# Optimization experiments

Measured on AMD Instinct MI355X. Metric: run time of the kernel, lower is better.

Reference implementation:

```python
import jax, jax.numpy as jnp
import numpy as np

C = 128
SHAPE = (1, C, 48, 48, 48)  # (N, C, D, H, W)
FILTERS = (1, 3, 3, 3, 1)
INIT_SCALE = 10.0
TAIL_MASS = 1e-9
LIKELIHOOD_BOUND = 1e-9


def setup_inputs() -> dict:
    key = jax.random.key(0)
    ks = jax.random.split(key, 8)
    x = jax.random.normal(ks[0], SHAPE, jnp.float32) * 3.0
    noise = jax.random.uniform(ks[1], SHAPE, jnp.float32)  # shifted to [-0.5,0.5) inside reference
    scale = INIT_SCALE ** (1.0 / (len(FILTERS) - 1))
    inp = {"x": x, "noise": noise}
    for i in range(4):
        init_m = float(np.log(np.expm1(1.0 / scale / FILTERS[i + 1])))
        inp[f"m{i}"] = jnp.full((C, FILTERS[i + 1], FILTERS[i]), init_m, jnp.float32)
        inp[f"b{i}"] = jax.random.uniform(ks[2 + i], (C, FILTERS[i + 1], 1), jnp.float32, -0.5, 0.5)
        if i < 3:
            inp[f"f{i}"] = jnp.zeros((C, FILTERS[i + 1], 1), jnp.float32)
    # quantiles init: [-init_scale, 0, init_scale] per channel, shape (C,1,3)
    inp["quantiles"] = jnp.tile(
        jnp.array([[[-INIT_SCALE, 0.0, INIT_SCALE]]], jnp.float32), (C, 1, 1)
    )
    return inp


def _logits_cumulative(z, mats, biases, factors, stop_gradient=False):
    # z: (C, 1, B); per-channel tiny 4-layer CDF MLP
    sg = jax.lax.stop_gradient if stop_gradient else (lambda t: t)
    for i in range(4):
        m = sg(jax.nn.softplus(mats[i]))          # (C, f_out, f_in)
        z = jnp.matmul(m, z) + sg(biases[i])      # (C, f_out, B)
        if i < 3:
            z = z + sg(jnp.tanh(factors[i])) * jnp.tanh(z)
    return z


def reference(x, noise, m0, m1, m2, m3, b0, b1, b2, b3, f0, f1, f2, quantiles):
    mats = [m0, m1, m2, m3]
    biases = [b0, b1, b2, b3]
    factors = [f0, f1, f2]

    # quantize_mode == 'noise': additive uniform(-0.5, 0.5) noise
    outputs = x + (noise - 0.5)

    n, c, d, h, w = outputs.shape
    z = jnp.transpose(outputs, (1, 0, 2, 3, 4)).reshape(c, 1, -1)  # (C,1,B)
    lower = _logits_cumulative(z - 0.5, mats, biases, factors)
    upper = _logits_cumulative(z + 0.5, mats, biases, factors)
    sign = -jax.lax.stop_gradient(jnp.sign(lower + upper))
    likelihood = jnp.abs(jax.nn.sigmoid(sign * upper) - jax.nn.sigmoid(sign * lower))
    likelihood = jnp.transpose(likelihood.reshape(c, n, d, h, w), (1, 0, 2, 3, 4))
    likelihood = jnp.maximum(likelihood, LIKELIHOOD_BOUND)  # Low_bound forward

    t = float(np.log(2.0 / TAIL_MASS - 1.0))
    target = jnp.array([-t, 0.0, t], jnp.float32)
    logits_q = _logits_cumulative(quantiles, mats, biases, factors, stop_gradient=True)
    quantiles_loss = jnp.sum(jnp.abs(logits_q - target))

    return outputs, likelihood, quantiles_loss
```

## Files before the change

kernel.cpp:

```cpp
#include <hip/hip_runtime.h>
#include <math.h>

#define NCH      128
#define SPATIAL  110592
#define NV4      3538944
#define CV4      27648
#define THREADS  256
#define GRID     2048

#define QT 21.416413017506358f

typedef float v4f __attribute__((ext_vector_type(4)));

__device__ __forceinline__ float frcp(float x){ return __builtin_amdgcn_rcpf(x); }
__device__ __forceinline__ float ftanh(float x){ return 1.0f - 2.0f*frcp(__expf(2.0f*x) + 1.0f); }
__device__ __forceinline__ float fsig(float x){ return frcp(1.0f + __expf(-x)); }
__device__ __forceinline__ float fsoftplus(float x){ return fmaxf(x, 0.0f) + log1pf(__expf(-fabsf(x))); }

struct Params {
    float w0[3], w1[9], w2[9], w3[3];
    float t0[3], t1[3], t2[3];
    float B0[3], B1[3], B2[3], B3;
};

__device__ __forceinline__ Params load_params(int c,
    const float* __restrict__ m0, const float* __restrict__ b0, const float* __restrict__ f0,
    const float* __restrict__ m1, const float* __restrict__ b1, const float* __restrict__ f1,
    const float* __restrict__ m2, const float* __restrict__ b2, const float* __restrict__ f2,
    const float* __restrict__ m3, const float* __restrict__ b3)
{
    Params P;
    #pragma unroll
    for (int k=0;k<3;k++) P.w0[k]=fsoftplus(m0[c*3+k]);
    #pragma unroll
    for (int k=0;k<9;k++) P.w1[k]=fsoftplus(m1[c*9+k]);
    #pragma unroll
    for (int k=0;k<9;k++) P.w2[k]=fsoftplus(m2[c*9+k]);
    #pragma unroll
    for (int k=0;k<3;k++) P.w3[k]=fsoftplus(m3[c*3+k]);
    #pragma unroll
    for (int k=0;k<3;k++) P.t0[k]=ftanh(f0[c*3+k]);
    #pragma unroll
    for (int k=0;k<3;k++) P.t1[k]=ftanh(f1[c*3+k]);
    #pragma unroll
    for (int k=0;k<3;k++) P.t2[k]=ftanh(f2[c*3+k]);
    #pragma unroll
    for (int k=0;k<3;k++) P.B0[k]=b0[c*3+k];
    #pragma unroll
    for (int k=0;k<3;k++) P.B1[k]=b1[c*3+k];
    #pragma unroll
    for (int k=0;k<3;k++) P.B2[k]=b2[c*3+k];
    P.B3 = b3[c];
    return P;
}

template<bool USE_F>
__device__ __forceinline__ float eval_mlp(float z, const Params& P){
    float h0 = fmaf(P.w0[0], z, P.B0[0]);
    float h1 = fmaf(P.w0[1], z, P.B0[1]);
    float h2 = fmaf(P.w0[2], z, P.B0[2]);
    if (USE_F){
        h0 = fmaf(P.t0[0], ftanh(h0), h0);
        h1 = fmaf(P.t0[1], ftanh(h1), h1);
        h2 = fmaf(P.t0[2], ftanh(h2), h2);
    }
    float g0 = fmaf(P.w1[0],h0, fmaf(P.w1[1],h1, fmaf(P.w1[2],h2, P.B1[0])));
    float g1 = fmaf(P.w1[3],h0, fmaf(P.w1[4],h1, fmaf(P.w1[5],h2, P.B1[1])));
    float g2 = fmaf(P.w1[6],h0, fmaf(P.w1[7],h1, fmaf(P.w1[8],h2, P.B1[2])));
    if (USE_F){
        g0 = fmaf(P.t1[0], ftanh(g0), g0);
        g1 = fmaf(P.t1[1], ftanh(g1), g1);
        g2 = fmaf(P.t1[2], ftanh(g2), g2);
    }
    h0 = fmaf(P.w2[0],g0, fmaf(P.w2[1],g1, fmaf(P.w2[2],g2, P.B2[0])));
    h1 = fmaf(P.w2[3],g0, fmaf(P.w2[4],g1, fmaf(P.w2[5],g2, P.B2[1])));
    h2 = fmaf(P.w2[6],g0, fmaf(P.w2[7],g1, fmaf(P.w2[8],g2, P.B2[2])));
    if (USE_F){
        h0 = fmaf(P.t2[0], ftanh(h0), h0);
        h1 = fmaf(P.t2[1], ftanh(h1), h1);
        h2 = fmaf(P.t2[2], ftanh(h2), h2);
    }
    return fmaf(P.w3[0],h0, fmaf(P.w3[1],h1, fmaf(P.w3[2],h2, P.B3)));
}

__device__ __forceinline__ float lik_from_logits(float lo, float hi){
    float su = lo + hi;
    float s  = (su > 0.0f) ? -1.0f : ((su < 0.0f) ? 1.0f : 0.0f);
    float a  = fsig(s*hi);
    float b  = fsig(s*lo);
    return fmaxf(fabsf(a - b), 1e-9f);
}

__global__ __launch_bounds__(384) void eb_prep(
    const float* __restrict__ m0, const float* __restrict__ b0, const float* __restrict__ f0,
    const float* __restrict__ m1, const float* __restrict__ b1, const float* __restrict__ f1,
    const float* __restrict__ m2, const float* __restrict__ b2, const float* __restrict__ f2,
    const float* __restrict__ m3, const float* __restrict__ b3,
    const float* __restrict__ q, float* __restrict__ loss,
    float2* __restrict__ ab, int* __restrict__ flag)
{
    const int tid = threadIdx.x;
    const int c = tid / 3;
    const int j = tid - c*3;

    Params P = load_params(c, m0,b0,f0, m1,b1,f1, m2,b2,f2, m3,b3);

    bool anyf = false;
    #pragma unroll
    for (int k=0;k<3;k++)
        anyf = anyf || (P.t0[k]!=0.0f) || (P.t1[k]!=0.0f) || (P.t2[k]!=0.0f);

    __shared__ int sf;
    if (tid == 0) sf = 0;
    __syncthreads();
    if (anyf) sf = 1;

    float z      = q[c*3 + j];
    float logit  = eval_mlp<true>(z, P);
    float target = (j==0) ? -QT : ((j==1) ? 0.0f : QT);
    float diff   = fabsf(logit - target);

    #pragma unroll
    for (int off = 32; off > 0; off >>= 1)
        diff += __shfl_down(diff, off, 64);

    __shared__ float red[6];
    if ((tid & 63) == 0) red[tid >> 6] = diff;
    __syncthreads();
    if (tid == 0){
        float s = 0.0f;
        #pragma unroll
        for (int i = 0; i < 6; i++) s += red[i];
        *loss = s;
        *flag = sf;
    }

    if (j == 0){
        float B = eval_mlp<false>(0.0f, P);
        float A = eval_mlp<false>(1.0f, P) - B;
        ab[c] = make_float2(A, B - 0.5f*A);
    }
}

__global__ __launch_bounds__(THREADS) void eb_main(
    const float* __restrict__ x, const float* __restrict__ noise,
    const float* __restrict__ m0, const float* __restrict__ b0, const float* __restrict__ f0,
    const float* __restrict__ m1, const float* __restrict__ b1, const float* __restrict__ f1,
    const float* __restrict__ m2, const float* __restrict__ b2, const float* __restrict__ f2,
    const float* __restrict__ m3, const float* __restrict__ b3,
    const float2* __restrict__ ab, const int* __restrict__ flag,
    float* __restrict__ out, float* __restrict__ lik)
{
    __shared__ float sA[NCH], sBl[NCH];
    __shared__ int sflag;
    const int tid = threadIdx.x;
    if (tid < NCH){ float2 v = ab[tid]; sA[tid] = v.x; sBl[tid] = v.y; }
    if (tid == 0) sflag = *flag;
    __syncthreads();
    const bool use_f = (sflag != 0);

    const v4f* __restrict__ x4 = (const v4f*)x;
    const v4f* __restrict__ n4 = (const v4f*)noise;
    v4f* __restrict__ o4 = (v4f*)out;
    v4f* __restrict__ l4 = (v4f*)lik;

    int i = blockIdx.x*THREADS + tid;
    const int stride = GRID*THREADS;

    if (!use_f){
        v4f xa = x4[i], na = n4[i];
        while (true){
            const int inext = i + stride;
            const bool vnext = inext < NV4;
            v4f xb, nb;
            if (vnext){ xb = x4[inext]; nb = n4[inext]; }

            const int c = i / CV4;
            const float A  = sA[c];
            const float Bl = sBl[c];

            v4f ov, lv;
            #pragma unroll
            for (int e = 0; e < 4; ++e){
                float o  = xa[e] + na[e] - 0.5f;
                float lo = fmaf(A, o, Bl);
                float hi = lo + A;
                ov[e] = o;
                lv[e] = lik_from_logits(lo, hi);
            }
            __builtin_nontemporal_store(ov, o4 + i);
            __builtin_nontemporal_store(lv, l4 + i);

            if (!vnext) break;
            i = inext; xa = xb; na = nb;
        }
    } else {
        for (; i < NV4; i += stride){
            const int c = i / CV4;
            Params P = load_params(c, m0,b0,f0, m1,b1,f1, m2,b2,f2, m3,b3);
            v4f xv = x4[i], nv = n4[i];
            v4f ov, lv;
            #pragma unroll
            for (int e = 0; e < 4; ++e){
                float o  = xv[e] + nv[e] - 0.5f;
                float lo = eval_mlp<true>(o - 0.5f, P);
                float hi = eval_mlp<true>(o + 0.5f, P);
                ov[e] = o;
                lv[e] = lik_from_logits(lo, hi);
            }
            __builtin_nontemporal_store(ov, o4 + i);
            __builtin_nontemporal_store(lv, l4 + i);
        }
    }
}

extern "C" void kernel_launch(void* const* d_in, const int* in_sizes, int n_in,
                              void* d_out, int out_size, void* d_ws, size_t ws_size,
                              hipStream_t stream) {
    const float* x  = (const float*)d_in[0];
    const float* nz = (const float*)d_in[1];
    const float* m0 = (const float*)d_in[2];
    const float* b0 = (const float*)d_in[3];
    const float* f0 = (const float*)d_in[4];
    const float* m1 = (const float*)d_in[5];
    const float* b1 = (const float*)d_in[6];
    const float* f1 = (const float*)d_in[7];
    const float* m2 = (const float*)d_in[8];
    const float* b2 = (const float*)d_in[9];
    const float* f2 = (const float*)d_in[10];
    const float* m3 = (const float*)d_in[11];
    const float* b3 = (const float*)d_in[12];
    const float* qq = (const float*)d_in[13];

    float* out  = (float*)d_out;
    float* lik  = out + (size_t)NCH*SPATIAL;
    float* loss = lik + (size_t)NCH*SPATIAL;

    float2* ab  = (float2*)d_ws;
    int*   flag = (int*)((char*)d_ws + NCH*sizeof(float2));

    eb_prep<<<1, 384, 0, stream>>>(m0,b0,f0, m1,b1,f1, m2,b2,f2, m3,b3, qq, loss, ab, flag);
    eb_main<<<GRID, THREADS, 0, stream>>>(x, nz, m0,b0,f0, m1,b1,f1, m2,b2,f2, m3,b3,
                                          ab, flag, out, lik);
}
```

Baseline: 231.4 us.

## Issue all tile loads up front with fixed per-block channel mapping

Replaces the grid-stride loop with a fixed 8-tile-per-thread scheme over 1728 blocks. All 16 vector loads are issued before any compute to raise memory-level parallelism. Each block's channels are known at compile time from the block index, which removes the shared-memory staging of per-channel coefficients and the block barrier. It raises register pressure and hardcodes the shape-dependent index mapping.

After: 238.4 us. 1.03x slower.

```diff
diff --git a/kernel.cpp b/kernel.cpp
--- a/kernel.cpp
+++ b/kernel.cpp
@@ -6,7 +6,9 @@
 #define NV4      3538944
 #define CV4      27648
 #define THREADS  256
-#define GRID     2048
+#define GRID     1728
+#define KTILES   8
+#define STRIDE   442368
 
 #define QT 21.416413017506358f
 
@@ -151,58 +153,57 @@
     const float2* __restrict__ ab, const int* __restrict__ flag,
     float* __restrict__ out, float* __restrict__ lik)
 {
-    __shared__ float sA[NCH], sBl[NCH];
-    __shared__ int sflag;
-    const int tid = threadIdx.x;
-    if (tid < NCH){ float2 v = ab[tid]; sA[tid] = v.x; sBl[tid] = v.y; }
-    if (tid == 0) sflag = *flag;
-    __syncthreads();
-    const bool use_f = (sflag != 0);
+    const int tid   = threadIdx.x;
+    const int cbase = blockIdx.x / 108;
+    const int i0    = blockIdx.x*THREADS + tid;
 
     const v4f* __restrict__ x4 = (const v4f*)x;
     const v4f* __restrict__ n4 = (const v4f*)noise;
     v4f* __restrict__ o4 = (v4f*)out;
     v4f* __restrict__ l4 = (v4f*)lik;
 
-    int i = blockIdx.x*THREADS + tid;
-    const int stride = GRID*THREADS;
+    const bool use_f = (*flag != 0);
 
     if (!use_f){
-        v4f xa = x4[i], na = n4[i];
-        while (true){
-            const int inext = i + stride;
-            const bool vnext = inext < NV4;
-            v4f xb, nb;
-            if (vnext){ xb = x4[inext]; nb = n4[inext]; }
-
-            const int c = i / CV4;
-            const float A  = sA[c];
-            const float Bl = sBl[c];
-
+        float A[KTILES], Bl[KTILES];
+        #pragma unroll
+        for (int k = 0; k < KTILES; ++k){
+            float2 v = ab[cbase + 16*k];
+            A[k] = v.x; Bl[k] = v.y;
+        }
+
+        v4f xv[KTILES], nv[KTILES];
+        #pragma unroll
+        for (int k = 0; k < KTILES; ++k){
+            xv[k] = x4[i0 + k*STRIDE];
+            nv[k] = n4[i0 + k*STRIDE];
+        }
+
+        #pragma unroll
+        for (int k = 0; k < KTILES; ++k){
             v4f ov, lv;
             #pragma unroll
             for (int e = 0; e < 4; ++e){
-                float o  = xa[e] + na[e] - 0.5f;
-                float lo = fmaf(A, o, Bl);
-                float hi = lo + A;
+                float o  = xv[k][e] + nv[k][e] - 0.5f;
+                float lo = fmaf(A[k], o, Bl[k]);
+                float hi = lo + A[k];
                 ov[e] = o;
                 lv[e] = lik_from_logits(lo, hi);
             }
-            __builtin_nontemporal_store(ov, o4 + i);
-            __builtin_nontemporal_store(lv, l4 + i);
-
-            if (!vnext) break;
-            i = inext; xa = xb; na = nb;
+            __builtin_nontemporal_store(ov, o4 + i0 + k*STRIDE);
+            __builtin_nontemporal_store(lv, l4 + i0 + k*STRIDE);
         }
     } else {
-        for (; i < NV4; i += stride){
-            const int c = i / CV4;
+        #pragma unroll
+        for (int k = 0; k < KTILES; ++k){
+            const int i = i0 + k*STRIDE;
+            const int c = cbase + 16*k;
             Params P = load_params(c, m0,b0,f0, m1,b1,f1, m2,b2,f2, m3,b3);
-            v4f xv = x4[i], nv = n4[i];
+            v4f xvv = x4[i], nvv = n4[i];
             v4f ov, lv;
             #pragma unroll
             for (int e = 0; e < 4; ++e){
-                float o  = xv[e] + nv[e] - 0.5f;
+                float o  = xvv[e] + nvv[e] - 0.5f;
                 float lo = eval_mlp<true>(o - 0.5f, P);
                 float hi = eval_mlp<true>(o + 0.5f, P);
                 ov[e] = o;
```
